# Kernel tuning notes

Hardware: AMD Instinct MI355X
Metric: run time of the kernel (lower is better)

The kernel has to match this reference:

```python
import jax, jax.numpy as jnp
import numpy as np

D = 768      # num_hiddens (hardcoded by dense1/dense2/ln in the source)
H = 12       # num_heads
NEG = -1000000.0
EPS = 1e-5


def setup_inputs() -> dict:
    key = jax.random.key(0)
    ks = jax.random.split(key, 14)
    B, Lq, Lk = 8, 1024, 1024
    s = 0.02
    return {
        "queries": jax.random.normal(ks[0], (B, Lq, D), dtype=jnp.float32),
        "keys":    jax.random.normal(ks[1], (B, Lk, D), dtype=jnp.float32),
        "values":  jax.random.normal(ks[2], (B, Lk, D), dtype=jnp.float32),
        # binary padding masks; count_nonzero along axis 1 gives valid lens
        "mask_1": jax.random.randint(ks[3], (B, Lk), 0, 2, dtype=jnp.int32),
        "mask_2": jax.random.randint(ks[4], (B, Lq), 0, 2, dtype=jnp.int32),
        # projection weights stored as [in, out] (torch Linear is y = x @ W.T)
        "Wq": jax.random.normal(ks[5], (D, D), dtype=jnp.float32) * s,
        "Wk": jax.random.normal(ks[6], (D, D), dtype=jnp.float32) * s,
        "Wv": jax.random.normal(ks[7], (D, D), dtype=jnp.float32) * s,
        "Wo": jax.random.normal(ks[8], (D, D), dtype=jnp.float32) * s,
        "d1_w": jax.random.normal(ks[9], (D, D), dtype=jnp.float32) * s,
        "d1_b": jnp.zeros((D,), dtype=jnp.float32),
        "d2_w": jax.random.normal(ks[10], (D, D), dtype=jnp.float32) * s,
        "d2_b": jnp.zeros((D,), dtype=jnp.float32),
        "ln_g": jnp.ones((D,), dtype=jnp.float32),
        "ln_b": jnp.zeros((D,), dtype=jnp.float32),
    }


def _cross_att(queries, keys, values, mask_1, mask_2,
               Wq, Wk, Wv, Wo, d1_w, d1_b, d2_w, d2_b, ln_g, ln_b):
    B, Lq, _ = queries.shape
    Lk = keys.shape[1]
    hd = D // H
    # project + split heads: [B, H, L, hd]
    q = (queries @ Wq).reshape(B, Lq, H, hd).transpose(0, 2, 1, 3)
    k = (keys    @ Wk).reshape(B, Lk, H, hd).transpose(0, 2, 1, 3)
    v = (values  @ Wv).reshape(B, Lk, H, hd).transpose(0, 2, 1, 3)
    scores = jnp.einsum('bhqd,bhkd->bhqk', q, k) / jnp.sqrt(jnp.float32(hd))
    # dual-axis prefix mask from nonzero counts
    vl1 = jnp.sum(mask_1 != 0, axis=1)  # [B], masks key axis
    vl2 = jnp.sum(mask_2 != 0, axis=1)  # [B], masks query axis
    col_ok = jnp.arange(Lk)[None, None, None, :] < vl1[:, None, None, None]
    row_ok = jnp.arange(Lq)[None, None, :, None] < vl2[:, None, None, None]
    scores = jnp.where(col_ok & row_ok, scores, NEG)
    attn = jax.nn.softmax(scores, axis=-1)
    out = jnp.einsum('bhqk,bhkd->bhqd', attn, v)
    out = out.transpose(0, 2, 1, 3).reshape(B, Lq, D)
    mha = out @ Wo
    ffn = jax.nn.relu(mha @ d1_w + d1_b) @ d2_w + d2_b
    x = ffn + mha  # dropout is identity in eval
    mu = jnp.mean(x, axis=-1, keepdims=True)
    var = jnp.mean(jnp.square(x - mu), axis=-1, keepdims=True)
    return (x - mu) / jnp.sqrt(var + EPS) * ln_g + ln_b


def reference(queries, keys, values, mask_1, mask_2,
              Wq, Wk, Wv, Wo, d1_w, d1_b, d2_w, d2_b, ln_g, ln_b):
    return _cross_att(queries, keys, values, mask_1, mask_2,
                      Wq, Wk, Wv, Wo, d1_w, d1_b, d2_w, d2_b, ln_g, ln_b)
```

## Files before the change

kernel.cpp:

```cpp
#include <hip/hip_runtime.h>
#include <hip/hip_bf16.h>
#include <type_traits>

#define DM   768
#define NH   12
#define HD   64
#define BATCH 8
#define SEQ  1024
#define NROWS (BATCH * SEQ)

typedef short bf16x8 __attribute__((ext_vector_type(8)));
typedef float f32x4 __attribute__((ext_vector_type(4)));

__device__ inline unsigned short f2b(float x) {
    union { float f; unsigned int u; } v; v.f = x;
    return (unsigned short)((v.u + 0x8000u) >> 16);
}
__device__ inline unsigned int f2b2(float lo, float hi) {
    union { float f; unsigned int u; } a, b; a.f = lo; b.f = hi;
    return __builtin_amdgcn_perm(b.u + 0x8000u, a.u + 0x8000u, 0x07060302u);
}
__device__ inline float b2f(unsigned short u) {
    union { float f; unsigned int x; } v; v.x = ((unsigned int)u) << 16;
    return v.f;
}

__device__ inline void gld16(const unsigned short* g, unsigned short* l) {
    __builtin_amdgcn_global_load_lds(
        (const __attribute__((address_space(1))) unsigned int*)g,
        (__attribute__((address_space(3))) unsigned int*)l, 16, 0, 0);
}

__global__ __launch_bounds__(256) void prep_kernel(const float* __restrict__ w0,
                                                   const float* __restrict__ w1,
                                                   const float* __restrict__ w2,
                                                   const float* __restrict__ w3,
                                                   const float* __restrict__ w4,
                                                   const float* __restrict__ w5,
                                                   unsigned short* __restrict__ wt,
                                                   const float* __restrict__ qin,
                                                   const float* __restrict__ kin,
                                                   const float* __restrict__ vin,
                                                   unsigned short* __restrict__ oq,
                                                   unsigned short* __restrict__ ok,
                                                   unsigned short* __restrict__ ov) {
    const int z = blockIdx.z;
    const int t = threadIdx.x;

    if (z >= 6) {
        const int linear = (z - 6) * 576 + blockIdx.y * 24 + blockIdx.x;
        const int g = linear / 3072;
        const int r = linear % 3072;
        const float* src = (g == 0) ? qin : (g == 1) ? kin : vin;
        unsigned short* dst = (g == 0) ? oq : (g == 1) ? ok : ov;
        const size_t i = ((size_t)r * 256 + t) * 8;
        float4 f0 = ((const float4*)(src + i))[0];
        float4 f1 = ((const float4*)(src + i))[1];
        uint4 p;
        p.x = f2b2(f0.x, f0.y); p.y = f2b2(f0.z, f0.w);
        p.z = f2b2(f1.x, f1.y); p.w = f2b2(f1.z, f1.w);
        *(uint4*)(dst + i) = p;
        return;
    }

    {
        __shared__ float tile[32][33];
        const float* W = (z == 0) ? w0 : (z == 1) ? w1 : (z == 2) ? w2
                       : (z == 3) ? w3 : (z == 4) ? w4 : w5;
        unsigned short* Wt = wt + (size_t)z * DM * DM;
        const int n0 = blockIdx.x * 32;
        const int k0 = blockIdx.y * 32;
        const int tx = t & 31;
        const int ty = t >> 5;
#pragma unroll
        for (int r = 0; r < 4; ++r)
            tile[ty + 8 * r][tx] = W[(size_t)(k0 + ty + 8 * r) * DM + n0 + tx];
        __syncthreads();
#pragma unroll
        for (int r = 0; r < 4; ++r)
            Wt[(size_t)(n0 + ty + 8 * r) * DM + k0 + tx] = f2b(tile[tx][ty + 8 * r]);
    }
}

__global__ __launch_bounds__(256) void qkv_gemm(const unsigned short* __restrict__ aq,
                                                const unsigned short* __restrict__ akk,
                                                const unsigned short* __restrict__ av_,
                                                unsigned short* __restrict__ wt,
                                                unsigned short* __restrict__ c0,
                                                unsigned short* __restrict__ c1,
                                                unsigned short* __restrict__ c2,
                                                const float* __restrict__ wof,
                                                const float* __restrict__ d1wf,
                                                const int* __restrict__ m1,
                                                const int* __restrict__ m2,
                                                int* __restrict__ lens) {
    __shared__ __align__(16) unsigned short As[128][32];
    __shared__ __align__(16) unsigned short Ws[128][32];

    const int t = threadIdx.x;

    if (blockIdx.y >= 18) {
        const int id = (blockIdx.y - 18) * 64 + blockIdx.x;
        if (id < 144) {
            unsigned short (*As40)[40] = (unsigned short(*)[40])&As[0][0];
            unsigned short (*Bs40)[40] = (unsigned short(*)[40])&Ws[0][0];
            unsigned short* out = wt + (size_t)6 * DM * DM;
            const int mb = (id % 12) * 64;
            const int nb = (id / 12) * 64;
            const int wid = t >> 6, lane = t & 63;
            const int quad = lane >> 4, l16 = lane & 15;
            const int bk = t >> 3, bn = (t & 7) * 8;
            const int am = t >> 2, ak = (t & 3) * 8;

            f32x4 acc[4];
#pragma unroll
            for (int c = 0; c < 4; ++c) acc[c] = (f32x4){0.f, 0.f, 0.f, 0.f};

            for (int j0 = 0; j0 < DM; j0 += 32) {
                {
                    const float* s = &d1wf[(size_t)(j0 + bk) * DM + mb + bn];
                    float4 f0 = ((const float4*)s)[0];
                    float4 f1 = ((const float4*)s)[1];
                    As40[bn + 0][bk] = f2b(f0.x); As40[bn + 1][bk] = f2b(f0.y);
                    As40[bn + 2][bk] = f2b(f0.z); As40[bn + 3][bk] = f2b(f0.w);
                    As40[bn + 4][bk] = f2b(f1.x); As40[bn + 5][bk] = f2b(f1.y);
                    As40[bn + 6][bk] = f2b(f1.z); As40[bn + 7][bk] = f2b(f1.w);
                }
                {
                    const float* s = &wof[(size_t)(nb + am) * DM + j0 + ak];
                    float4 f0 = ((const float4*)s)[0];
                    float4 f1 = ((const float4*)s)[1];
                    uint4 p;
                    p.x = f2b2(f0.x, f0.y); p.y = f2b2(f0.z, f0.w);
                    p.z = f2b2(f1.x, f1.y); p.w = f2b2(f1.z, f1.w);
                    *(uint4*)&Bs40[am][ak] = p;
                }
                __syncthreads();
                bf16x8 a2 = *(const bf16x8*)&As40[16 * wid + l16][quad * 8];
#pragma unroll
                for (int c = 0; c < 4; ++c) {
                    bf16x8 b2v = *(const bf16x8*)&Bs40[16 * c + l16][quad * 8];
                    acc[c] = __builtin_amdgcn_mfma_f32_16x16x32_bf16(a2, b2v, acc[c], 0, 0, 0);
                }
                __syncthreads();
            }
#pragma unroll
            for (int c = 0; c < 4; ++c) {
                const int col = nb + 16 * c + l16;
#pragma unroll
                for (int r = 0; r < 4; ++r) {
                    const int row = mb + 16 * wid + quad * 4 + r;
                    out[(size_t)row * DM + col] = f2b(acc[c][r]);
                }
            }
        } else if (id < 160) {
            const int bid = id - 144;
            int* redi = (int*)&As[0][0];
            const int b = bid & 7;
            const int* m = (bid < 8) ? m1 : m2;
            int cnt = 0;
            for (int i = t; i < SEQ; i += 256) cnt += (m[b * SEQ + i] != 0) ? 1 : 0;
            redi[t] = cnt;
            __syncthreads();
            for (int off = 128; off > 0; off >>= 1) {
                if (t < off) redi[t] += redi[t + off];
                __syncthreads();
            }
            if (t == 0) lens[bid] = redi[0];
        }
        return;
    }

    const int g = blockIdx.y / 6;
    const int m0 = blockIdx.x * 128;
    const int n0 = (blockIdx.y % 6) * 128;
    const unsigned short* A = (g == 0) ? aq : (g == 1) ? akk : av_;
    const unsigned short* Wt = wt + (size_t)g * DM * DM;
    unsigned short* C = (g == 0) ? c0 : (g == 1) ? c1 : c2;
    const float cs = (g == 0) ? 0.18033688f : 1.0f;

    const int w = t >> 6, lane = t & 63;
    const int quad = lane >> 4, l16 = lane & 15;
    const int wm = w & 1, wn = w >> 1;
    const int srow = 16 * w + (lane >> 2);
    const int scol = 8 * ((lane & 3) ^ ((lane >> 3) & 3));
    const int swr = (quad ^ ((l16 >> 1) & 3)) * 8;

    f32x4 acc[4][4];
#pragma unroll
    for (int i = 0; i < 4; ++i)
#pragma unroll
        for (int j = 0; j < 4; ++j) acc[i][j] = (f32x4){0.f, 0.f, 0.f, 0.f};

    for (int k0 = 0; k0 < DM; k0 += 32) {
#pragma unroll
        for (int j = 0; j < 2; ++j) {
            gld16(&A[(size_t)(m0 + srow + 64 * j) * DM + k0 + scol],
                  &As[16 * w + 64 * j][0]);
            gld16(&Wt[(size_t)(n0 + srow + 64 * j) * DM + k0 + scol],
                  &Ws[16 * w + 64 * j][0]);
        }
        __syncthreads();

        bf16x8 av[4], bv[4];
#pragma unroll
        for (int i = 0; i < 4; ++i)
            av[i] = *(const bf16x8*)&As[wm * 64 + 16 * i + l16][swr];
#pragma unroll
        for (int i = 0; i < 4; ++i)
            bv[i] = *(const bf16x8*)&Ws[wn * 64 + 16 * i + l16][swr];
#pragma unroll
        for (int i = 0; i < 4; ++i)
#pragma unroll
            for (int j = 0; j < 4; ++j)
                acc[i][j] = __builtin_amdgcn_mfma_f32_16x16x32_bf16(bv[j], av[i], acc[i][j], 0, 0, 0);
        __syncthreads();
    }

#pragma unroll
    for (int i = 0; i < 4; ++i) {
        const int tok = m0 + wm * 64 + 16 * i + l16;
        unsigned short* crow = &C[(size_t)tok * DM + n0 + wn * 64 + quad * 4];
#pragma unroll
        for (int j = 0; j < 4; ++j) {
            uint2 pr;
            pr.x = f2b2(acc[i][j][0] * cs, acc[i][j][1] * cs);
            pr.y = f2b2(acc[i][j][2] * cs, acc[i][j][3] * cs);
            *(uint2*)(crow + 16 * j) = pr;
        }
    }
}

__global__ __launch_bounds__(256) void vpart_kernel(const unsigned short* __restrict__ v,
                                                    float* __restrict__ vp) {
    __shared__ float red[4][64];
    const int t = threadIdx.x;
    const int bh = blockIdx.x;
    const int chunk = blockIdx.y;
    const int b = bh / NH, h = bh % NH;
    const int d = t & 63, rg = t >> 6;
    const unsigned short* base =
        v + (size_t)(b * SEQ + chunk * 128 + rg * 32) * DM + h * HD + d;
    float s = 0.0f;
#pragma unroll 4
    for (int i = 0; i < 32; ++i) s += b2f(base[(size_t)i * DM]);
    red[rg][d] = s;
    __syncthreads();
    if (rg == 0)
        vp[((size_t)bh * 8 + chunk) * 64 + d] = red[0][d] + red[1][d] + red[2][d] + red[3][d];
}

template <typename CT>
__global__ __launch_bounds__(256) void gemm_bf(const unsigned short* __restrict__ A,
                                               const unsigned short* __restrict__ Wt,
                                               CT* __restrict__ C,
                                               const float* __restrict__ bias,
                                               const unsigned short* __restrict__ res,
                                               int relu) {
    __shared__ __align__(16) unsigned short As[128][32];
    __shared__ __align__(16) unsigned short Ws[128][32];

    const int t = threadIdx.x;
    const int m0 = blockIdx.x * 128;
    const int n0 = blockIdx.y * 128;
    const int w = t >> 6, lane = t & 63;
    const int quad = lane >> 4, l16 = lane & 15;
    const int wm = w & 1, wn = w >> 1;
    const int srow = 16 * w + (lane >> 2);
    const int scol = 8 * ((lane & 3) ^ ((lane >> 3) & 3));
    const int swr = (quad ^ ((l16 >> 1) & 3)) * 8;

    f32x4 acc[4][4];
#pragma unroll
    for (int i = 0; i < 4; ++i)
#pragma unroll
        for (int j = 0; j < 4; ++j) acc[i][j] = (f32x4){0.f, 0.f, 0.f, 0.f};

    for (int k0 = 0; k0 < DM; k0 += 32) {
#pragma unroll
        for (int j = 0; j < 2; ++j) {
            gld16(&A[(size_t)(m0 + srow + 64 * j) * DM + k0 + scol],
                  &As[16 * w + 64 * j][0]);
            gld16(&Wt[(size_t)(n0 + srow + 64 * j) * DM + k0 + scol],
                  &Ws[16 * w + 64 * j][0]);
        }
        __syncthreads();

        bf16x8 av[4], bv[4];
#pragma unroll
        for (int i = 0; i < 4; ++i)
            av[i] = *(const bf16x8*)&As[wm * 64 + 16 * i + l16][swr];
#pragma unroll
        for (int i = 0; i < 4; ++i)
            bv[i] = *(const bf16x8*)&Ws[wn * 64 + 16 * i + l16][swr];
#pragma unroll
        for (int i = 0; i < 4; ++i)
#pragma unroll
            for (int j = 0; j < 4; ++j)
                acc[i][j] = __builtin_amdgcn_mfma_f32_16x16x32_bf16(bv[j], av[i], acc[i][j], 0, 0, 0);
        __syncthreads();
    }

#pragma unroll
    for (int i = 0; i < 4; ++i) {
        const int tok = m0 + wm * 64 + 16 * i + l16;
#pragma unroll
        for (int j = 0; j < 4; ++j) {
            const int fb = n0 + wn * 64 + 16 * j + quad * 4;
            float cv0 = acc[i][j][0], cv1 = acc[i][j][1];
            float cv2 = acc[i][j][2], cv3 = acc[i][j][3];
            if (bias) {
                const float4 bb = *(const float4*)&bias[fb];
                cv0 += bb.x; cv1 += bb.y; cv2 += bb.z; cv3 += bb.w;
            }
            if (relu) {
                cv0 = fmaxf(cv0, 0.0f); cv1 = fmaxf(cv1, 0.0f);
                cv2 = fmaxf(cv2, 0.0f); cv3 = fmaxf(cv3, 0.0f);
            }
            if (res) {
                const uint2 rr = *(const uint2*)&res[(size_t)tok * DM + fb];
                cv0 += b2f((unsigned short)(rr.x & 0xffffu));
                cv1 += b2f((unsigned short)(rr.x >> 16));
                cv2 += b2f((unsigned short)(rr.y & 0xffffu));
                cv3 += b2f((unsigned short)(rr.y >> 16));
            }
            if constexpr (std::is_same<CT, float>::value) {
                float4 o4; o4.x = cv0; o4.y = cv1; o4.z = cv2; o4.w = cv3;
                *(float4*)&C[(size_t)tok * DM + fb] = o4;
            } else {
                uint2 pr;
                pr.x = f2b2(cv0, cv1);
                pr.y = f2b2(cv2, cv3);
                *(uint2*)&C[(size_t)tok * DM + fb] = pr;
            }
        }
    }
}

__global__ __launch_bounds__(256) void gemm_mh(const unsigned short* __restrict__ A,
                                               const unsigned short* __restrict__ wt,
                                               unsigned short* __restrict__ cm,
                                               unsigned short* __restrict__ ch,
                                               const float* __restrict__ d1b) {
    __shared__ __align__(16) unsigned short As[128][32];
    __shared__ __align__(16) unsigned short Ws[128][32];

    const int t = threadIdx.x;
    const int unit = blockIdx.y / 6;
    const unsigned short* Wt = wt + (size_t)(unit ? 6 : 3) * DM * DM;
    unsigned short* C = unit ? ch : cm;
    const int m0 = blockIdx.x * 128;
    const int n0 = (blockIdx.y % 6) * 128;
    const int w = t >> 6, lane = t & 63;
    const int quad = lane >> 4, l16 = lane & 15;
    const int wm = w & 1, wn = w >> 1;
    const int srow = 16 * w + (lane >> 2);
    const int scol = 8 * ((lane & 3) ^ ((lane >> 3) & 3));
    const int swr = (quad ^ ((l16 >> 1) & 3)) * 8;

    f32x4 acc[4][4];
#pragma unroll
    for (int i = 0; i < 4; ++i)
#pragma unroll
        for (int j = 0; j < 4; ++j) acc[i][j] = (f32x4){0.f, 0.f, 0.f, 0.f};

    for (int k0 = 0; k0 < DM; k0 += 32) {
#pragma unroll
        for (int j = 0; j < 2; ++j) {
            gld16(&A[(size_t)(m0 + srow + 64 * j) * DM + k0 + scol],
                  &As[16 * w + 64 * j][0]);
            gld16(&Wt[(size_t)(n0 + srow + 64 * j) * DM + k0 + scol],
                  &Ws[16 * w + 64 * j][0]);
        }
        __syncthreads();

        bf16x8 av[4], bv[4];
#pragma unroll
        for (int i = 0; i < 4; ++i)
            av[i] = *(const bf16x8*)&As[wm * 64 + 16 * i + l16][swr];
#pragma unroll
        for (int i = 0; i < 4; ++i)
            bv[i] = *(const bf16x8*)&Ws[wn * 64 + 16 * i + l16][swr];
#pragma unroll
        for (int i = 0; i < 4; ++i)
#pragma unroll
            for (int j = 0; j < 4; ++j)
                acc[i][j] = __builtin_amdgcn_mfma_f32_16x16x32_bf16(bv[j], av[i], acc[i][j], 0, 0, 0);
        __syncthreads();
    }

#pragma unroll
    for (int i = 0; i < 4; ++i) {
        const int tok = m0 + wm * 64 + 16 * i + l16;
#pragma unroll
        for (int j = 0; j < 4; ++j) {
            const int fb = n0 + wn * 64 + 16 * j + quad * 4;
            float cv0 = acc[i][j][0], cv1 = acc[i][j][1];
            float cv2 = acc[i][j][2], cv3 = acc[i][j][3];
            if (unit) {
                const float4 bb = *(const float4*)&d1b[fb];
                cv0 = fmaxf(cv0 + bb.x, 0.0f);
                cv1 = fmaxf(cv1 + bb.y, 0.0f);
                cv2 = fmaxf(cv2 + bb.z, 0.0f);
                cv3 = fmaxf(cv3 + bb.w, 0.0f);
            }
            uint2 pr;
            pr.x = f2b2(cv0, cv1);
            pr.y = f2b2(cv2, cv3);
            *(uint2*)&C[(size_t)tok * DM + fb] = pr;
        }
    }
}

__global__ __launch_bounds__(256) void attn_mfma(const unsigned short* Q,
                                                 const unsigned short* __restrict__ K,
                                                 const unsigned short* __restrict__ V,
                                                 unsigned short* O,
                                                 const int* __restrict__ lens,
                                                 const float* __restrict__ vp) {
    __shared__ __align__(16) unsigned short Ks[64][72];
    __shared__ __align__(16) unsigned short Vt[64][72];
    __shared__ __align__(16) unsigned short Ps[4][16][72];

    const int t = threadIdx.x;
    const int bid = blockIdx.x;
    const int q0 = (bid & 15) * 64;
    const int h = (bid >> 4) % NH;
    const int b = bid / (16 * NH);
    const int vl1 = lens[b];
    const int vl2 = lens[8 + b];
    const int wid = t >> 6;
    const int lane = t & 63;
    const int quad = lane >> 4;
    const int l16 = lane & 15;
    const size_t vpb = (size_t)(b * NH + h) * 8 * 64;

    if (q0 >= vl2 || vl1 == 0) {
        float vm[4];
#pragma unroll
        for (int ct = 0; ct < 4; ++ct) {
            float s = 0.0f;
#pragma unroll
            for (int c = 0; c < 8; ++c) s += vp[vpb + (size_t)c * 64 + 16 * ct + l16];
            vm[ct] = s * (1.0f / 1024.0f);
        }
#pragma unroll
        for (int r = 0; r < 4; ++r) {
            const size_t row = (size_t)(b * SEQ + q0 + 16 * wid + quad * 4 + r);
#pragma unroll
            for (int ct = 0; ct < 4; ++ct)
                O[row * DM + h * HD + 16 * ct + l16] = f2b(vm[ct]);
        }
        return;
    }

    bf16x8 qa0, qa1;
    {
        const unsigned short* qp =
            &Q[(size_t)(b * SEQ + q0 + 16 * wid + l16) * DM + h * HD + quad * 8];
        qa0 = *(const bf16x8*)qp;
        qa1 = *(const bf16x8*)(qp + 32);
    }

    f32x4 o[4];
#pragma unroll
    for (int ct = 0; ct < 4; ++ct) o[ct] = (f32x4){0.f, 0.f, 0.f, 0.f};
    float suml[4];
    bool rbad[4];
#pragma unroll
    for (int r = 0; r < 4; ++r) {
        suml[r] = 0.0f;
        rbad[r] = (q0 + 16 * wid + quad * 4 + r) >= vl2;
    }

    const int nt = (vl1 + 63) >> 6;

    const int kkr = t >> 3;
    const int khc = (t & 7) * 8;
    const unsigned short* kbase = &K[(size_t)(b * SEQ) * DM + h * HD];
    const unsigned short* vbase = &V[(size_t)(b * SEQ) * DM + h * HD];

    uint4 kr0 = *(const uint4*)&kbase[(size_t)kkr * DM + khc];
    uint4 kr1 = *(const uint4*)&kbase[(size_t)(kkr + 32) * DM + khc];
    uint4 vr0 = *(const uint4*)&vbase[(size_t)lane * DM + wid * 16];
    uint4 vr1 = *(const uint4*)&vbase[(size_t)lane * DM + wid * 16 + 8];

    const int k2 = l16 >> 2;

    for (int tile = 0; tile < nt; ++tile) {
        const int c0 = tile * 64;
        *(uint4*)&Ks[kkr][khc] = kr0;
        *(uint4*)&Ks[kkr + 32][khc] = kr1;
        {
            union { uint4 u; unsigned short s[8]; } va, vb;
            va.u = vr0; vb.u = vr1;
#pragma unroll
            for (int j = 0; j < 8; ++j) Vt[wid * 16 + j][lane] = va.s[j];
#pragma unroll
            for (int j = 0; j < 8; ++j) Vt[wid * 16 + 8 + j][lane] = vb.s[j];
        }
        __syncthreads();

        if (tile < nt - 1) {
            const int c1 = c0 + 64;
            kr0 = *(const uint4*)&kbase[(size_t)(c1 + kkr) * DM + khc];
            kr1 = *(const uint4*)&kbase[(size_t)(c1 + kkr + 32) * DM + khc];
            vr0 = *(const uint4*)&vbase[(size_t)(c1 + lane) * DM + wid * 16];
            vr1 = *(const uint4*)&vbase[(size_t)(c1 + lane) * DM + wid * 16 + 8];
        }

        f32x4 s[4];
#pragma unroll
        for (int ct = 0; ct < 4; ++ct) {
            f32x4 acc = (f32x4){0.f, 0.f, 0.f, 0.f};
            bf16x8 b0v = *(const bf16x8*)&Ks[16 * ct + l16][quad * 8];
            bf16x8 b1v = *(const bf16x8*)&Ks[16 * ct + l16][32 + quad * 8];
            acc = __builtin_amdgcn_mfma_f32_16x16x32_bf16(qa0, b0v, acc, 0, 0, 0);
            acc = __builtin_amdgcn_mfma_f32_16x16x32_bf16(qa1, b1v, acc, 0, 0, 0);
            s[ct] = acc;
        }
#pragma unroll
        for (int ct = 0; ct < 4; ++ct) {
            const bool kok = (c0 + 16 * ct + l16) < vl1;
#pragma unroll
            for (int r = 0; r < 4; ++r) {
                float e = __builtin_amdgcn_exp2f(s[ct][r]);
                float p = kok ? e : 0.0f;
                s[ct][r] = p;
                suml[r] += p;
            }
        }
#pragma unroll
        for (int ct = 0; ct < 4; ++ct) {
            const int gidx = 2 * ct + (l16 >> 3);
            const int c = l16 & 7;
            const int gs = (gidx ^ quad) * 8 + c;
#pragma unroll
            for (int r = 0; r < 4; ++r)
                Ps[wid][quad * 4 + r][gs] = f2b(s[ct][r]);
        }
        bf16x8 pa0 = *(const bf16x8*)&Ps[wid][l16][(quad ^ k2) * 8];
        bf16x8 pa1 = *(const bf16x8*)&Ps[wid][l16][((4 + quad) ^ k2) * 8];
#pragma unroll
        for (int ct = 0; ct < 4; ++ct) {
            bf16x8 vb0 = *(const bf16x8*)&Vt[16 * ct + l16][quad * 8];
            bf16x8 vb1 = *(const bf16x8*)&Vt[16 * ct + l16][32 + quad * 8];
            o[ct] = __builtin_amdgcn_mfma_f32_16x16x32_bf16(pa0, vb0, o[ct], 0, 0, 0);
            o[ct] = __builtin_amdgcn_mfma_f32_16x16x32_bf16(pa1, vb1, o[ct], 0, 0, 0);
        }
        __syncthreads();
    }

#pragma unroll
    for (int d = 1; d < 16; d <<= 1) {
#pragma unroll
        for (int r = 0; r < 4; ++r) suml[r] += __shfl_xor(suml[r], d, 64);
    }

    float vm[4];
    if (rbad[0] || rbad[3]) {
#pragma unroll
        for (int ct = 0; ct < 4; ++ct) {
            float s = 0.0f;
#pragma unroll
            for (int c = 0; c < 8; ++c) s += vp[vpb + (size_t)c * 64 + 16 * ct + l16];
            vm[ct] = s * (1.0f / 1024.0f);
        }
    }
#pragma unroll
    for (int r = 0; r < 4; ++r) {
        const float inv = 1.0f / suml[r];
        const size_t row = (size_t)(b * SEQ + q0 + 16 * wid + quad * 4 + r);
#pragma unroll
        for (int ct = 0; ct < 4; ++ct) {
            const float val = rbad[r] ? vm[ct] : o[ct][r] * inv;
            O[row * DM + h * HD + 16 * ct + l16] = f2b(val);
        }
    }
}

__global__ __launch_bounds__(256) void ln_kernel(float* __restrict__ X,
                                                 const float* __restrict__ g,
                                                 const float* __restrict__ bvec) {
    __shared__ float red[256];
    const int row = blockIdx.x;
    const int t = threadIdx.x;
    float* xr = X + (size_t)row * DM;
    float x0 = xr[t];
    float x1 = xr[t + 256];
    float x2 = xr[t + 512];
    red[t] = x0 + x1 + x2;
    __syncthreads();
    for (int off = 128; off > 0; off >>= 1) {
        if (t < off) red[t] += red[t + off];
        __syncthreads();
    }
    float mu = red[0] * (1.0f / 768.0f);
    __syncthreads();
    float d0 = x0 - mu, d1 = x1 - mu, d2 = x2 - mu;
    red[t] = d0 * d0 + d1 * d1 + d2 * d2;
    __syncthreads();
    for (int off = 128; off > 0; off >>= 1) {
        if (t < off) red[t] += red[t + off];
        __syncthreads();
    }
    float rstd = rsqrtf(red[0] * (1.0f / 768.0f) + 1e-5f);
    xr[t]       = d0 * rstd * g[t]       + bvec[t];
    xr[t + 256] = d1 * rstd * g[t + 256] + bvec[t + 256];
    xr[t + 512] = d2 * rstd * g[t + 512] + bvec[t + 512];
}

extern "C" void kernel_launch(void* const* d_in, const int* in_sizes, int n_in,
                              void* d_out, int out_size, void* d_ws, size_t ws_size,
                              hipStream_t stream) {
    const float* queries = (const float*)d_in[0];
    const float* keys    = (const float*)d_in[1];
    const float* values  = (const float*)d_in[2];
    const int* mask1 = (const int*)d_in[3];
    const int* mask2 = (const int*)d_in[4];
    const float* Wq  = (const float*)d_in[5];
    const float* Wk  = (const float*)d_in[6];
    const float* Wv  = (const float*)d_in[7];
    const float* Wo  = (const float*)d_in[8];
    const float* d1w = (const float*)d_in[9];
    const float* d1b = (const float*)d_in[10];
    const float* d2w = (const float*)d_in[11];
    const float* d2b = (const float*)d_in[12];
    const float* lng = (const float*)d_in[13];
    const float* lnb = (const float*)d_in[14];

    char* ws = (char*)d_ws;
    int* lens = (int*)ws;
    float* vp = (float*)(ws + 256);
    const size_t VP = (size_t)96 * 8 * 64 * sizeof(float);
    const size_t NB = (size_t)NROWS * DM * sizeof(unsigned short);
    const size_t WT = (size_t)DM * DM;
    unsigned short* b0 = (unsigned short*)(ws + 256 + VP);
    unsigned short* b1 = (unsigned short*)(ws + 256 + VP + NB);
    unsigned short* b2 = (unsigned short*)(ws + 256 + VP + 2 * NB);
    unsigned short* wt = (unsigned short*)(ws + 256 + VP + 3 * NB);
    unsigned short* aq = (unsigned short*)(ws + 256 + VP + 3 * NB + 7 * WT * sizeof(unsigned short));
    unsigned short* ak = aq + (size_t)NROWS * DM;
    unsigned short* av = ak + (size_t)NROWS * DM;
    float* xout = (float*)d_out;

    prep_kernel<<<dim3(24, 24, 22), 256, 0, stream>>>(Wq, Wk, Wv, Wo, d1w, d2w,
                                                      wt, queries, keys, values,
                                                      aq, ak, av);

    qkv_gemm<<<dim3(64, 21), 256, 0, stream>>>(aq, ak, av, wt, b0, b1, b2,
                                               Wo, d1w, mask1, mask2, lens);

    vpart_kernel<<<dim3(96, 8), 256, 0, stream>>>(b2, vp);

    attn_mfma<<<16 * NH * BATCH, 256, 0, stream>>>(b0, b1, b2, b0, lens, vp);

    gemm_mh<<<dim3(64, 12), 256, 0, stream>>>(b0, wt, b1, b2, d1b);

    gemm_bf<float><<<dim3(64, 6), 256, 0, stream>>>(b2, wt + 5 * WT, xout, d2b, b1, 0);

    ln_kernel<<<NROWS, 256, 0, stream>>>(xout, lng, lnb);
}
```

Baseline: 316.0 us.

## Double-buffer LDS in GEMMs and prefetch weight-fold loads into registers

```diff
diff --git a/kernel.cpp b/kernel.cpp
--- a/kernel.cpp
+++ b/kernel.cpp
@@ -49,17 +49,23 @@
 
     if (z >= 6) {
         const int linear = (z - 6) * 576 + blockIdx.y * 24 + blockIdx.x;
-        const int g = linear / 3072;
-        const int r = linear % 3072;
+        const int c0 = linear * 2;
+        const int g = c0 / 3072;
+        const int r = c0 % 3072;
         const float* src = (g == 0) ? qin : (g == 1) ? kin : vin;
         unsigned short* dst = (g == 0) ? oq : (g == 1) ? ok : ov;
         const size_t i = ((size_t)r * 256 + t) * 8;
         float4 f0 = ((const float4*)(src + i))[0];
         float4 f1 = ((const float4*)(src + i))[1];
+        float4 f2 = ((const float4*)(src + i + 2048))[0];
+        float4 f3 = ((const float4*)(src + i + 2048))[1];
         uint4 p;
         p.x = f2b2(f0.x, f0.y); p.y = f2b2(f0.z, f0.w);
         p.z = f2b2(f1.x, f1.y); p.w = f2b2(f1.z, f1.w);
         *(uint4*)(dst + i) = p;
+        p.x = f2b2(f2.x, f2.y); p.y = f2b2(f2.z, f2.w);
+        p.z = f2b2(f3.x, f3.y); p.w = f2b2(f3.z, f3.w);
+        *(uint4*)(dst + i + 2048) = p;
         return;
     }
 
@@ -94,16 +100,16 @@
                                                 const int* __restrict__ m1,
                                                 const int* __restrict__ m2,
                                                 int* __restrict__ lens) {
-    __shared__ __align__(16) unsigned short As[128][32];
-    __shared__ __align__(16) unsigned short Ws[128][32];
+    __shared__ __align__(16) unsigned short As[2][128][32];
+    __shared__ __align__(16) unsigned short Ws[2][128][32];
 
     const int t = threadIdx.x;
 
-    if (blockIdx.y >= 18) {
-        const int id = (blockIdx.y - 18) * 64 + blockIdx.x;
+    if (blockIdx.y < 3) {
+        const int id = blockIdx.y * 64 + blockIdx.x;
         if (id < 144) {
-            unsigned short (*As40)[40] = (unsigned short(*)[40])&As[0][0];
-            unsigned short (*Bs40)[40] = (unsigned short(*)[40])&Ws[0][0];
+            unsigned short (*As40)[40] = (unsigned short(*)[40])&As[0][0][0];
+            unsigned short (*Bs40)[40] = (unsigned short(*)[40])&Ws[0][0][0];
             unsigned short* out = wt + (size_t)6 * DM * DM;
             const int mb = (id % 12) * 64;
             const int nb = (id / 12) * 64;
@@ -116,26 +122,33 @@
 #pragma unroll
             for (int c = 0; c < 4; ++c) acc[c] = (f32x4){0.f, 0.f, 0.f, 0.f};
 
+            const float* sA = &d1wf[(size_t)bk * DM + mb + bn];
+            const float* sB = &wof[(size_t)(nb + am) * DM + ak];
+            float4 a0 = ((const float4*)sA)[0];
+            float4 a1 = ((const float4*)sA)[1];
+            float4 bb0 = ((const float4*)sB)[0];
+            float4 bb1 = ((const float4*)sB)[1];
+
             for (int j0 = 0; j0 < DM; j0 += 32) {
+                As40[bn + 0][bk] = f2b(a0.x); As40[bn + 1][bk] = f2b(a0.y);
+                As40[bn + 2][bk] = f2b(a0.z); As40[bn + 3][bk] = f2b(a0.w);
+                As40[bn + 4][bk] = f2b(a1.x); As40[bn + 5][bk] = f2b(a1.y);
+                As40[bn + 6][bk] = f2b(a1.z); As40[bn + 7][bk] = f2b(a1.w);
                 {
-                    const float* s = &d1wf[(size_t)(j0 + bk) * DM + mb + bn];
-                    float4 f0 = ((const float4*)s)[0];
-                    float4 f1 = ((const float4*)s)[1];
-                    As40[bn + 0][bk] = f2b(f0.x); As40[bn + 1][bk] = f2b(f0.y);
-                    As40[bn + 2][bk] = f2b(f0.z); As40[bn + 3][bk] = f2b(f0.w);
-                    As40[bn + 4][bk] = f2b(f1.x); As40[bn + 5][bk] = f2b(f1.y);
-                    As40[bn + 6][bk] = f2b(f1.z); As40[bn + 7][bk] = f2b(f1.w);
-                }
-                {
-                    const float* s = &wof[(size_t)(nb + am) * DM + j0 + ak];
-                    float4 f0 = ((const float4*)s)[0];
-                    float4 f1 = ((const float4*)s)[1];
                     uint4 p;
-                    p.x = f2b2(f0.x, f0.y); p.y = f2b2(f0.z, f0.w);
-                    p.z = f2b2(f1.x, f1.y); p.w = f2b2(f1.z, f1.w);
+                    p.x = f2b2(bb0.x, bb0.y); p.y = f2b2(bb0.z, bb0.w);
+                    p.z = f2b2(bb1.x, bb1.y); p.w = f2b2(bb1.z, bb1.w);
                     *(uint4*)&Bs40[am][ak] = p;
                 }
                 __syncthreads();
+                if (j0 + 32 < DM) {
+                    const float* nA = &d1wf[(size_t)(j0 + 32 + bk) * DM + mb + bn];
+                    const float* nB = &wof[(size_t)(nb + am) * DM + j0 + 32 + ak];
+                    a0 = ((const float4*)nA)[0];
+                    a1 = ((const float4*)nA)[1];
+                    bb0 = ((const float4*)nB)[0];
+                    bb1 = ((const float4*)nB)[1];
+                }
                 bf16x8 a2 = *(const bf16x8*)&As40[16 * wid + l16][quad * 8];
 #pragma unroll
                 for (int c = 0; c < 4; ++c) {
@@ -155,7 +168,7 @@
             }
         } else if (id < 160) {
             const int bid = id - 144;
-            int* redi = (int*)&As[0][0];
+            int* redi = (int*)&As[0][0][0];
             const int b = bid & 7;
             const int* m = (bid < 8) ? m1 : m2;
             int cnt = 0;
@@ -171,9 +184,10 @@
         return;
     }
 
-    const int g = blockIdx.y / 6;
+    const int yy = blockIdx.y - 3;
+    const int g = yy / 6;
     const int m0 = blockIdx.x * 128;
-    const int n0 = (blockIdx.y % 6) * 128;
+    const int n0 = (yy % 6) * 128;
     const unsigned short* A = (g == 0) ? aq : (g == 1) ? akk : av_;
     const unsigned short* Wt = wt + (size_t)g * DM * DM;
     unsigned short* C = (g == 0) ? c0 : (g == 1) ? c1 : c2;
@@ -192,23 +206,31 @@
 #pragma unroll
         for (int j = 0; j < 4; ++j) acc[i][j] = (f32x4){0.f, 0.f, 0.f, 0.f};
 
+#pragma unroll
+    for (int j = 0; j < 2; ++j) {
+        gld16(&A[(size_t)(m0 + srow + 64 * j) * DM + scol], &As[0][16 * w + 64 * j][0]);
+        gld16(&Wt[(size_t)(n0 + srow + 64 * j) * DM + scol], &Ws[0][16 * w + 64 * j][0]);
+    }
+    __syncthreads();
+
     for (int k0 = 0; k0 < DM; k0 += 32) {
-#pragma unroll
-        for (int j = 0; j < 2; ++j) {
-            gld16(&A[(size_t)(m0 + srow + 64 * j) * DM + k0 + scol],
-                  &As[16 * w + 64 * j][0]);
-            gld16(&Wt[(size_t)(n0 + srow + 64 * j) * DM + k0 + scol],
-                  &Ws[16 * w + 64 * j][0]);
-        }
-        __syncthreads();
-
+        const int cur = (k0 >> 5) & 1;
+        if (k0 + 32 < DM) {
+#pragma unroll
+            for (int j = 0; j < 2; ++j) {
+                gld16(&A[(size_t)(m0 + srow + 64 * j) * DM + k0 + 32 + scol],
+                      &As[cur ^ 1][16 * w + 64 * j][0]);
+                gld16(&Wt[(size_t)(n0 + srow + 64 * j) * DM + k0 + 32 + scol],
+                      &Ws[cur ^ 1][16 * w + 64 * j][0]);
+            }
+        }
         bf16x8 av[4], bv[4];
 #pragma unroll
         for (int i = 0; i < 4; ++i)
-            av[i] = *(const bf16x8*)&As[wm * 64 + 16 * i + l16][swr];
-#pragma unroll
-        for (int i = 0; i < 4; ++i)
-            bv[i] = *(const bf16x8*)&Ws[wn * 64 + 16 * i + l16][swr];
+            av[i] = *(const bf16x8*)&As[cur][wm * 64 + 16 * i + l16][swr];
+#pragma unroll
+        for (int i = 0; i < 4; ++i)
+            bv[i] = *(const bf16x8*)&Ws[cur][wn * 64 + 16 * i + l16][swr];
 #pragma unroll
         for (int i = 0; i < 4; ++i)
 #pragma unroll
@@ -257,8 +279,8 @@
                                                const float* __restrict__ bias,
                                                const unsigned short* __restrict__ res,
                                                int relu) {
-    __shared__ __align__(16) unsigned short As[128][32];
-    __shared__ __align__(16) unsigned short Ws[128][32];
+    __shared__ __align__(16) unsigned short As[2][128][32];
+    __shared__ __align__(16) unsigned short Ws[2][128][32];
 
     const int t = threadIdx.x;
     const int m0 = blockIdx.x * 128;
@@ -276,23 +298,31 @@
 #pragma unroll
         for (int j = 0; j < 4; ++j) acc[i][j] = (f32x4){0.f, 0.f, 0.f, 0.f};
 
+#pragma unroll
+    for (int j = 0; j < 2; ++j) {
+        gld16(&A[(size_t)(m0 + srow + 64 * j) * DM + scol], &As[0][16 * w + 64 * j][0]);
+        gld16(&Wt[(size_t)(n0 + srow + 64 * j) * DM + scol], &Ws[0][16 * w + 64 * j][0]);
+    }
+    __syncthreads();
+
     for (int k0 = 0; k0 < DM; k0 += 32) {
-#pragma unroll
-        for (int j = 0; j < 2; ++j) {
-            gld16(&A[(size_t)(m0 + srow + 64 * j) * DM + k0 + scol],
-                  &As[16 * w + 64 * j][0]);
-            gld16(&Wt[(size_t)(n0 + srow + 64 * j) * DM + k0 + scol],
-                  &Ws[16 * w + 64 * j][0]);
-        }
-        __syncthreads();
-
+        const int cur = (k0 >> 5) & 1;
+        if (k0 + 32 < DM) {
+#pragma unroll
+            for (int j = 0; j < 2; ++j) {
+                gld16(&A[(size_t)(m0 + srow + 64 * j) * DM + k0 + 32 + scol],
+                      &As[cur ^ 1][16 * w + 64 * j][0]);
+                gld16(&Wt[(size_t)(n0 + srow + 64 * j) * DM + k0 + 32 + scol],
+                      &Ws[cur ^ 1][16 * w + 64 * j][0]);
+            }
+        }
         bf16x8 av[4], bv[4];
 #pragma unroll
         for (int i = 0; i < 4; ++i)
-            av[i] = *(const bf16x8*)&As[wm * 64 + 16 * i + l16][swr];
-#pragma unroll
-        for (int i = 0; i < 4; ++i)
-            bv[i] = *(const bf16x8*)&Ws[wn * 64 + 16 * i + l16][swr];
+            av[i] = *(const bf16x8*)&As[cur][wm * 64 + 16 * i + l16][swr];
+#pragma unroll
+        for (int i = 0; i < 4; ++i)
+            bv[i] = *(const bf16x8*)&Ws[cur][wn * 64 + 16 * i + l16][swr];
 #pragma unroll
         for (int i = 0; i < 4; ++i)
 #pragma unroll
@@ -342,8 +372,8 @@
                                                unsigned short* __restrict__ cm,
                                                unsigned short* __restrict__ ch,
                                                const float* __restrict__ d1b) {
-    __shared__ __align__(16) unsigned short As[128][32];
-    __shared__ __align__(16) unsigned short Ws[128][32];
+    __shared__ __align__(16) unsigned short As[2][128][32];
+    __shared__ __align__(16) unsigned short Ws[2][128][32];
 
     const int t = threadIdx.x;
     const int unit = blockIdx.y / 6;
@@ -364,23 +394,31 @@
 #pragma unroll
         for (int j = 0; j < 4; ++j) acc[i][j] = (f32x4){0.f, 0.f, 0.f, 0.f};
 
+#pragma unroll
+    for (int j = 0; j < 2; ++j) {
+        gld16(&A[(size_t)(m0 + srow + 64 * j) * DM + scol], &As[0][16 * w + 64 * j][0]);
+        gld16(&Wt[(size_t)(n0 + srow + 64 * j) * DM + scol], &Ws[0][16 * w + 64 * j][0]);
+    }
+    __syncthreads();
+
     for (int k0 = 0; k0 < DM; k0 += 32) {
-#pragma unroll
-        for (int j = 0; j < 2; ++j) {
-            gld16(&A[(size_t)(m0 + srow + 64 * j) * DM + k0 + scol],
-                  &As[16 * w + 64 * j][0]);
-            gld16(&Wt[(size_t)(n0 + srow + 64 * j) * DM + k0 + scol],
-                  &Ws[16 * w + 64 * j][0]);
-        }
-        __syncthreads();
-
+        const int cur = (k0 >> 5) & 1;
+        if (k0 + 32 < DM) {
+#pragma unroll
+            for (int j = 0; j < 2; ++j) {
+                gld16(&A[(size_t)(m0 + srow + 64 * j) * DM + k0 + 32 + scol],
+                      &As[cur ^ 1][16 * w + 64 * j][0]);
+                gld16(&Wt[(size_t)(n0 + srow + 64 * j) * DM + k0 + 32 + scol],
+                      &Ws[cur ^ 1][16 * w + 64 * j][0]);
+            }
+        }
         bf16x8 av[4], bv[4];
 #pragma unroll
         for (int i = 0; i < 4; ++i)
-            av[i] = *(const bf16x8*)&As[wm * 64 + 16 * i + l16][swr];
-#pragma unroll
-        for (int i = 0; i < 4; ++i)
-            bv[i] = *(const bf16x8*)&Ws[wn * 64 + 16 * i + l16][swr];
+            av[i] = *(const bf16x8*)&As[cur][wm * 64 + 16 * i + l16][swr];
+#pragma unroll
+        for (int i = 0; i < 4; ++i)
+            bv[i] = *(const bf16x8*)&Ws[cur][wn * 64 + 16 * i + l16][swr];
 #pragma unroll
         for (int i = 0; i < 4; ++i)
 #pragma unroll
@@ -644,7 +682,7 @@
     unsigned short* av = ak + (size_t)NROWS * DM;
     float* xout = (float*)d_out;
 
-    prep_kernel<<<dim3(24, 24, 22), 256, 0, stream>>>(Wq, Wk, Wv, Wo, d1w, d2w,
+    prep_kernel<<<dim3(24, 24, 14), 256, 0, stream>>>(Wq, Wk, Wv, Wo, d1w, d2w,
                                                       wt, queries, keys, values,
                                                       aq, ak, av);
 
```

New measurement: 300.9 us. 4.8% less time.

## Triple-buffer GEMM main loop with async LDS loads and restructure Wo·d1 fusion

Applied to the files above, without the earlier changes.

```diff
diff --git a/kernel.cpp b/kernel.cpp
--- a/kernel.cpp
+++ b/kernel.cpp
@@ -29,6 +29,74 @@
     __builtin_amdgcn_global_load_lds(
         (const __attribute__((address_space(1))) unsigned int*)g,
         (__attribute__((address_space(3))) unsigned int*)l, 16, 0, 0);
+}
+
+__device__ __forceinline__ void mm_loop(const unsigned short* __restrict__ A,
+                                        const unsigned short* __restrict__ Wt,
+                                        int m0, int n0, int t,
+                                        unsigned short (*As)[128][32],
+                                        unsigned short (*Ws)[128][32],
+                                        f32x4 (&acc)[4][4]) {
+    const int w = t >> 6, lane = t & 63;
+    const int quad = lane >> 4, l16 = lane & 15;
+    const int wm = w & 1, wn = w >> 1;
+    const int srow = 16 * w + (lane >> 2);
+    const int scol = 8 * ((lane & 3) ^ ((lane >> 3) & 3));
+    const int swr = (quad ^ ((l16 >> 1) & 3)) * 8;
+
+#pragma unroll
+    for (int i = 0; i < 4; ++i)
+#pragma unroll
+        for (int j = 0; j < 4; ++j) acc[i][j] = (f32x4){0.f, 0.f, 0.f, 0.f};
+
+    const unsigned short* aP = &A[(size_t)(m0 + srow) * DM + scol];
+    const unsigned short* wP = &Wt[(size_t)(n0 + srow) * DM + scol];
+
+    auto stage = [&](int kk, int b) {
+#pragma unroll
+        for (int j = 0; j < 2; ++j) {
+            gld16(aP + (size_t)(64 * j) * DM + kk * 32, &As[b][16 * w + 64 * j][0]);
+            gld16(wP + (size_t)(64 * j) * DM + kk * 32, &Ws[b][16 * w + 64 * j][0]);
+        }
+    };
+    auto compute = [&](int b) {
+        bf16x8 av[4], bv[4];
+#pragma unroll
+        for (int i = 0; i < 4; ++i)
+            av[i] = *(const bf16x8*)&As[b][wm * 64 + 16 * i + l16][swr];
+#pragma unroll
+        for (int i = 0; i < 4; ++i)
+            bv[i] = *(const bf16x8*)&Ws[b][wn * 64 + 16 * i + l16][swr];
+#pragma unroll
+        for (int i = 0; i < 4; ++i)
+#pragma unroll
+            for (int j = 0; j < 4; ++j)
+                acc[i][j] = __builtin_amdgcn_mfma_f32_16x16x32_bf16(bv[j], av[i], acc[i][j], 0, 0, 0);
+    };
+
+    stage(0, 0);
+    stage(1, 1);
+    int b = 0;
+#pragma unroll 1
+    for (int k = 0; k < 22; ++k) {
+        int nb = b + 2; if (nb >= 3) nb -= 3;
+        stage(k + 2, nb);
+        asm volatile("s_waitcnt vmcnt(8)" ::: "memory");
+        __builtin_amdgcn_s_barrier();
+        compute(b);
+        asm volatile("" ::: "memory");
+        __builtin_amdgcn_s_barrier();
+        if (++b == 3) b = 0;
+    }
+    asm volatile("s_waitcnt vmcnt(4)" ::: "memory");
+    __builtin_amdgcn_s_barrier();
+    compute(b);
+    asm volatile("" ::: "memory");
+    __builtin_amdgcn_s_barrier();
+    if (++b == 3) b = 0;
+    asm volatile("s_waitcnt vmcnt(0)" ::: "memory");
+    __builtin_amdgcn_s_barrier();
+    compute(b);
 }
 
 __global__ __launch_bounds__(256) void prep_kernel(const float* __restrict__ w0,
@@ -38,6 +106,7 @@
                                                    const float* __restrict__ w4,
                                                    const float* __restrict__ w5,
                                                    unsigned short* __restrict__ wt,
+                                                   unsigned short* __restrict__ wob,
                                                    const float* __restrict__ qin,
                                                    const float* __restrict__ kin,
                                                    const float* __restrict__ vin,
@@ -49,17 +118,23 @@
 
     if (z >= 6) {
         const int linear = (z - 6) * 576 + blockIdx.y * 24 + blockIdx.x;
-        const int g = linear / 3072;
-        const int r = linear % 3072;
+        const int c0 = linear * 2;
+        const int g = c0 / 3072;
+        const int r = c0 % 3072;
         const float* src = (g == 0) ? qin : (g == 1) ? kin : vin;
         unsigned short* dst = (g == 0) ? oq : (g == 1) ? ok : ov;
         const size_t i = ((size_t)r * 256 + t) * 8;
         float4 f0 = ((const float4*)(src + i))[0];
         float4 f1 = ((const float4*)(src + i))[1];
+        float4 f2 = ((const float4*)(src + i + 2048))[0];
+        float4 f3 = ((const float4*)(src + i + 2048))[1];
         uint4 p;
         p.x = f2b2(f0.x, f0.y); p.y = f2b2(f0.z, f0.w);
         p.z = f2b2(f1.x, f1.y); p.w = f2b2(f1.z, f1.w);
         *(uint4*)(dst + i) = p;
+        p.x = f2b2(f2.x, f2.y); p.y = f2b2(f2.z, f2.w);
+        p.z = f2b2(f3.x, f3.y); p.w = f2b2(f3.z, f3.w);
+        *(uint4*)(dst + i + 2048) = p;
         return;
     }
 
@@ -72,9 +147,17 @@
         const int k0 = blockIdx.y * 32;
         const int tx = t & 31;
         const int ty = t >> 5;
-#pragma unroll
-        for (int r = 0; r < 4; ++r)
-            tile[ty + 8 * r][tx] = W[(size_t)(k0 + ty + 8 * r) * DM + n0 + tx];
+        float v[4];
+#pragma unroll
+        for (int r = 0; r < 4; ++r) {
+            v[r] = W[(size_t)(k0 + ty + 8 * r) * DM + n0 + tx];
+            tile[ty + 8 * r][tx] = v[r];
+        }
+        if (z == 3) {
+#pragma unroll
+            for (int r = 0; r < 4; ++r)
+                wob[(size_t)(k0 + ty + 8 * r) * DM + n0 + tx] = f2b(v[r]);
+        }
         __syncthreads();
 #pragma unroll
         for (int r = 0; r < 4; ++r)
@@ -86,76 +169,30 @@
                                                 const unsigned short* __restrict__ akk,
                                                 const unsigned short* __restrict__ av_,
                                                 unsigned short* __restrict__ wt,
+                                                const unsigned short* __restrict__ wob,
                                                 unsigned short* __restrict__ c0,
                                                 unsigned short* __restrict__ c1,
                                                 unsigned short* __restrict__ c2,
-                                                const float* __restrict__ wof,
-                                                const float* __restrict__ d1wf,
                                                 const int* __restrict__ m1,
                                                 const int* __restrict__ m2,
                                                 int* __restrict__ lens) {
-    __shared__ __align__(16) unsigned short As[128][32];
-    __shared__ __align__(16) unsigned short Ws[128][32];
+    __shared__ __align__(16) unsigned short As[3][128][32];
+    __shared__ __align__(16) unsigned short Ws[3][128][32];
 
     const int t = threadIdx.x;
-
-    if (blockIdx.y >= 18) {
-        const int id = (blockIdx.y - 18) * 64 + blockIdx.x;
-        if (id < 144) {
-            unsigned short (*As40)[40] = (unsigned short(*)[40])&As[0][0];
-            unsigned short (*Bs40)[40] = (unsigned short(*)[40])&Ws[0][0];
-            unsigned short* out = wt + (size_t)6 * DM * DM;
-            const int mb = (id % 12) * 64;
-            const int nb = (id / 12) * 64;
-            const int wid = t >> 6, lane = t & 63;
-            const int quad = lane >> 4, l16 = lane & 15;
-            const int bk = t >> 3, bn = (t & 7) * 8;
-            const int am = t >> 2, ak = (t & 3) * 8;
-
-            f32x4 acc[4];
-#pragma unroll
-            for (int c = 0; c < 4; ++c) acc[c] = (f32x4){0.f, 0.f, 0.f, 0.f};
-
-            for (int j0 = 0; j0 < DM; j0 += 32) {
-                {
-                    const float* s = &d1wf[(size_t)(j0 + bk) * DM + mb + bn];
-                    float4 f0 = ((const float4*)s)[0];
-                    float4 f1 = ((const float4*)s)[1];
-                    As40[bn + 0][bk] = f2b(f0.x); As40[bn + 1][bk] = f2b(f0.y);
-                    As40[bn + 2][bk] = f2b(f0.z); As40[bn + 3][bk] = f2b(f0.w);
-                    As40[bn + 4][bk] = f2b(f1.x); As40[bn + 5][bk] = f2b(f1.y);
-                    As40[bn + 6][bk] = f2b(f1.z); As40[bn + 7][bk] = f2b(f1.w);
-                }
-                {
-                    const float* s = &wof[(size_t)(nb + am) * DM + j0 + ak];
-                    float4 f0 = ((const float4*)s)[0];
-                    float4 f1 = ((const float4*)s)[1];
-                    uint4 p;
-                    p.x = f2b2(f0.x, f0.y); p.y = f2b2(f0.z, f0.w);
-                    p.z = f2b2(f1.x, f1.y); p.w = f2b2(f1.z, f1.w);
-                    *(uint4*)&Bs40[am][ak] = p;
-                }
-                __syncthreads();
-                bf16x8 a2 = *(const bf16x8*)&As40[16 * wid + l16][quad * 8];
-#pragma unroll
-                for (int c = 0; c < 4; ++c) {
-                    bf16x8 b2v = *(const bf16x8*)&Bs40[16 * c + l16][quad * 8];
-                    acc[c] = __builtin_amdgcn_mfma_f32_16x16x32_bf16(a2, b2v, acc[c], 0, 0, 0);
-                }
-                __syncthreads();
-            }
-#pragma unroll
-            for (int c = 0; c < 4; ++c) {
-                const int col = nb + 16 * c + l16;
-#pragma unroll
-                for (int r = 0; r < 4; ++r) {
-                    const int row = mb + 16 * wid + quad * 4 + r;
-                    out[(size_t)row * DM + col] = f2b(acc[c][r]);
-                }
-            }
-        } else if (id < 160) {
-            const int bid = id - 144;
-            int* redi = (int*)&As[0][0];
+    const size_t WT = (size_t)DM * DM;
+
+    const unsigned short* A;
+    const unsigned short* Wop;
+    unsigned short* C;
+    float cs;
+    int m0, n0;
+
+    if (blockIdx.y == 0) {
+        if (blockIdx.x >= 52) return;
+        if (blockIdx.x >= 36) {
+            const int bid = blockIdx.x - 36;
+            int* redi = (int*)&As[0][0][0];
             const int b = bid & 7;
             const int* m = (bid < 8) ? m1 : m2;
             int cnt = 0;
@@ -167,55 +204,31 @@
                 __syncthreads();
             }
             if (t == 0) lens[bid] = redi[0];
-        }
-        return;
-    }
-
-    const int g = blockIdx.y / 6;
-    const int m0 = blockIdx.x * 128;
-    const int n0 = (blockIdx.y % 6) * 128;
-    const unsigned short* A = (g == 0) ? aq : (g == 1) ? akk : av_;
-    const unsigned short* Wt = wt + (size_t)g * DM * DM;
-    unsigned short* C = (g == 0) ? c0 : (g == 1) ? c1 : c2;
-    const float cs = (g == 0) ? 0.18033688f : 1.0f;
+            return;
+        }
+        A = wt + 4 * WT;
+        Wop = wob;
+        C = wt + 6 * WT;
+        cs = 1.0f;
+        m0 = (blockIdx.x % 6) * 128;
+        n0 = (blockIdx.x / 6) * 128;
+    } else {
+        const int yy = blockIdx.y - 1;
+        const int g = yy / 6;
+        m0 = blockIdx.x * 128;
+        n0 = (yy % 6) * 128;
+        A = (g == 0) ? aq : (g == 1) ? akk : av_;
+        Wop = wt + (size_t)g * WT;
+        C = (g == 0) ? c0 : (g == 1) ? c1 : c2;
+        cs = (g == 0) ? 0.18033688f : 1.0f;
+    }
+
+    f32x4 acc[4][4];
+    mm_loop(A, Wop, m0, n0, t, As, Ws, acc);
 
     const int w = t >> 6, lane = t & 63;
     const int quad = lane >> 4, l16 = lane & 15;
     const int wm = w & 1, wn = w >> 1;
-    const int srow = 16 * w + (lane >> 2);
-    const int scol = 8 * ((lane & 3) ^ ((lane >> 3) & 3));
-    const int swr = (quad ^ ((l16 >> 1) & 3)) * 8;
-
-    f32x4 acc[4][4];
-#pragma unroll
-    for (int i = 0; i < 4; ++i)
-#pragma unroll
-        for (int j = 0; j < 4; ++j) acc[i][j] = (f32x4){0.f, 0.f, 0.f, 0.f};
-
-    for (int k0 = 0; k0 < DM; k0 += 32) {
-#pragma unroll
-        for (int j = 0; j < 2; ++j) {
-            gld16(&A[(size_t)(m0 + srow + 64 * j) * DM + k0 + scol],
-                  &As[16 * w + 64 * j][0]);
-            gld16(&Wt[(size_t)(n0 + srow + 64 * j) * DM + k0 + scol],
-                  &Ws[16 * w + 64 * j][0]);
-        }
-        __syncthreads();
-
-        bf16x8 av[4], bv[4];
-#pragma unroll
-        for (int i = 0; i < 4; ++i)
-            av[i] = *(const bf16x8*)&As[wm * 64 + 16 * i + l16][swr];
-#pragma unroll
-        for (int i = 0; i < 4; ++i)
-            bv[i] = *(const bf16x8*)&Ws[wn * 64 + 16 * i + l16][swr];
-#pragma unroll
-        for (int i = 0; i < 4; ++i)
-#pragma unroll
-            for (int j = 0; j < 4; ++j)
-                acc[i][j] = __builtin_amdgcn_mfma_f32_16x16x32_bf16(bv[j], av[i], acc[i][j], 0, 0, 0);
-        __syncthreads();
-    }
 
 #pragma unroll
     for (int i = 0; i < 4; ++i) {
@@ -257,49 +270,19 @@
                                                const float* __restrict__ bias,
                                                const unsigned short* __restrict__ res,
                                                int relu) {
-    __shared__ __align__(16) unsigned short As[128][32];
-    __shared__ __align__(16) unsigned short Ws[128][32];
+    __shared__ __align__(16) unsigned short As[3][128][32];
+    __shared__ __align__(16) unsigned short Ws[3][128][32];
 
     const int t = threadIdx.x;
     const int m0 = blockIdx.x * 128;
     const int n0 = blockIdx.y * 128;
+
+    f32x4 acc[4][4];
+    mm_loop(A, Wt, m0, n0, t, As, Ws, acc);
+
     const int w = t >> 6, lane = t & 63;
     const int quad = lane >> 4, l16 = lane & 15;
     const int wm = w & 1, wn = w >> 1;
-    const int srow = 16 * w + (lane >> 2);
-    const int scol = 8 * ((lane & 3) ^ ((lane >> 3) & 3));
-    const int swr = (quad ^ ((l16 >> 1) & 3)) * 8;
-
-    f32x4 acc[4][4];
-#pragma unroll
-    for (int i = 0; i < 4; ++i)
-#pragma unroll
-        for (int j = 0; j < 4; ++j) acc[i][j] = (f32x4){0.f, 0.f, 0.f, 0.f};
-
-    for (int k0 = 0; k0 < DM; k0 += 32) {
-#pragma unroll
-        for (int j = 0; j < 2; ++j) {
-            gld16(&A[(size_t)(m0 + srow + 64 * j) * DM + k0 + scol],
-                  &As[16 * w + 64 * j][0]);
-            gld16(&Wt[(size_t)(n0 + srow + 64 * j) * DM + k0 + scol],
-                  &Ws[16 * w + 64 * j][0]);
-        }
-        __syncthreads();
-
-        bf16x8 av[4], bv[4];
-#pragma unroll
-        for (int i = 0; i < 4; ++i)
-            av[i] = *(const bf16x8*)&As[wm * 64 + 16 * i + l16][swr];
-#pragma unroll
-        for (int i = 0; i < 4; ++i)
-            bv[i] = *(const bf16x8*)&Ws[wn * 64 + 16 * i + l16][swr];
-#pragma unroll
-        for (int i = 0; i < 4; ++i)
-#pragma unroll
-            for (int j = 0; j < 4; ++j)
-                acc[i][j] = __builtin_amdgcn_mfma_f32_16x16x32_bf16(bv[j], av[i], acc[i][j], 0, 0, 0);
-        __syncthreads();
-    }
 
 #pragma unroll
     for (int i = 0; i < 4; ++i) {
@@ -342,8 +325,8 @@
                                                unsigned short* __restrict__ cm,
                                                unsigned short* __restrict__ ch,
                                                const float* __restrict__ d1b) {
-    __shared__ __align__(16) unsigned short As[128][32];
-    __shared__ __align__(16) unsigned short Ws[128][32];
+    __shared__ __align__(16) unsigned short As[3][128][32];
+    __shared__ __align__(16) unsigned short Ws[3][128][32];
 
     const int t = threadIdx.x;
     const int unit = blockIdx.y / 6;
@@ -351,43 +334,13 @@
     unsigned short* C = unit ? ch : cm;
     const int m0 = blockIdx.x * 128;
     const int n0 = (blockIdx.y % 6) * 128;
+
+    f32x4 acc[4][4];
+    mm_loop(A, Wt, m0, n0, t, As, Ws, acc);
+
     const int w = t >> 6, lane = t & 63;
     const int quad = lane >> 4, l16 = lane & 15;
     const int wm = w & 1, wn = w >> 1;
-    const int srow = 16 * w + (lane >> 2);
-    const int scol = 8 * ((lane & 3) ^ ((lane >> 3) & 3));
-    const int swr = (quad ^ ((l16 >> 1) & 3)) * 8;
-
-    f32x4 acc[4][4];
-#pragma unroll
-    for (int i = 0; i < 4; ++i)
-#pragma unroll
-        for (int j = 0; j < 4; ++j) acc[i][j] = (f32x4){0.f, 0.f, 0.f, 0.f};
-
-    for (int k0 = 0; k0 < DM; k0 += 32) {
-#pragma unroll
-        for (int j = 0; j < 2; ++j) {
-            gld16(&A[(size_t)(m0 + srow + 64 * j) * DM + k0 + scol],
-                  &As[16 * w + 64 * j][0]);
-            gld16(&Wt[(size_t)(n0 + srow + 64 * j) * DM + k0 + scol],
-                  &Ws[16 * w + 64 * j][0]);
-        }
-        __syncthreads();
-
-        bf16x8 av[4], bv[4];
-#pragma unroll
-        for (int i = 0; i < 4; ++i)
-            av[i] = *(const bf16x8*)&As[wm * 64 + 16 * i + l16][swr];
-#pragma unroll
-        for (int i = 0; i < 4; ++i)
-            bv[i] = *(const bf16x8*)&Ws[wn * 64 + 16 * i + l16][swr];
-#pragma unroll
-        for (int i = 0; i < 4; ++i)
-#pragma unroll
-            for (int j = 0; j < 4; ++j)
-                acc[i][j] = __builtin_amdgcn_mfma_f32_16x16x32_bf16(bv[j], av[i], acc[i][j], 0, 0, 0);
-        __syncthreads();
-    }
 
 #pragma unroll
     for (int i = 0; i < 4; ++i) {
@@ -642,14 +595,15 @@
     unsigned short* aq = (unsigned short*)(ws + 256 + VP + 3 * NB + 7 * WT * sizeof(unsigned short));
     unsigned short* ak = aq + (size_t)NROWS * DM;
     unsigned short* av = ak + (size_t)NROWS * DM;
+    unsigned short* wob = av + (size_t)NROWS * DM;
     float* xout = (float*)d_out;
 
-    prep_kernel<<<dim3(24, 24, 22), 256, 0, stream>>>(Wq, Wk, Wv, Wo, d1w, d2w,
-                                                      wt, queries, keys, values,
+    prep_kernel<<<dim3(24, 24, 14), 256, 0, stream>>>(Wq, Wk, Wv, Wo, d1w, d2w,
+                                                      wt, wob, queries, keys, values,
                                                       aq, ak, av);
 
-    qkv_gemm<<<dim3(64, 21), 256, 0, stream>>>(aq, ak, av, wt, b0, b1, b2,
-                                               Wo, d1w, mask1, mask2, lens);
+    qkv_gemm<<<dim3(64, 19), 256, 0, stream>>>(aq, ak, av, wt, wob, b0, b1, b2,
+                                               mask1, mask2, lens);
 
     vpart_kernel<<<dim3(96, 8), 256, 0, stream>>>(b2, vp);
 
```

Result: no change. 311.6 us (-1.4%).
